# Optimization experiments

Hardware: AMD Instinct MI355X
Metric: run time of the kernel (lower is better)

## Reference

```python
import jax, jax.numpy as jnp
import numpy as np

EPS = 1e-4      # geomloss: eps = blur**p = 0.01**2
N_ITERS = 20    # fixed Sinkhorn iterations
UNI_T = 2.0     # uniformity temperature (Wang & Isola)


def _sqdist(x, y):
    # [N,D],[M,D] -> [N,M] squared euclidean distances
    return jnp.sum((x[:, None, :] - y[None, :, :]) ** 2, axis=-1)


def _cost(x, y):
    # geomloss p=2 cost: ||x-y||^2 / 2
    return 0.5 * _sqdist(x, y)


def _softmin(C, h):
    # f_i = -eps * log( (1/M) * sum_j exp((h_j - C_ij)/eps) )
    M = C.shape[1]
    lse = jax.nn.logsumexp((h[None, :] - C) / EPS, axis=1)
    return -EPS * (lse - jnp.log(jnp.float32(M)))


def _sinkhorn_potentials(C):
    # alternating log-domain Sinkhorn updates, uniform weights
    def body(carry, _):
        f, g = carry
        f = _softmin(C, g)
        g = _softmin(C.T, f)
        return (f, g), None
    init = (jnp.zeros(C.shape[0], C.dtype), jnp.zeros(C.shape[1], C.dtype))
    (f, g), _ = jax.lax.scan(body, init, None, length=N_ITERS)
    return f, g


def _sym_potential(C):
    # symmetric fixed-point for the debiasing terms OT_eps(a,a)
    def body(p, _):
        return 0.5 * (p + _softmin(C, p)), None
    p, _ = jax.lax.scan(body, jnp.zeros(C.shape[0], C.dtype), None, length=N_ITERS)
    return p


def sinkhorn_divergence(x, y):
    # debiased: S = OT(x,y) - 0.5*OT(x,x) - 0.5*OT(y,y); envelope-theorem grads
    Cxy = _cost(x, y)
    f_d, g_d = _sinkhorn_potentials(jax.lax.stop_gradient(Cxy))
    f = _softmin(Cxy, jax.lax.stop_gradient(g_d))          # final differentiable step
    g = _softmin(Cxy.T, jax.lax.stop_gradient(f_d))

    Cxx = _cost(x, x)
    px = _sym_potential(jax.lax.stop_gradient(Cxx))
    fx = _softmin(Cxx, jax.lax.stop_gradient(px))          # 0.5*OT(x,x) = mean(fx)

    Cyy = _cost(y, y)
    py = _sym_potential(jax.lax.stop_gradient(Cyy))
    fy = _softmin(Cyy, jax.lax.stop_gradient(py))

    return jnp.mean(f) + jnp.mean(g) - jnp.mean(fx) - jnp.mean(fy)


def uniformity(x):
    # log E_{i != j} [ exp(-t * ||x_i - x_j||^2) ]
    N = x.shape[0]
    D = _sqdist(x, x)
    D = D + jnp.diag(jnp.full((N,), jnp.inf, dtype=x.dtype))  # mask self-pairs
    return jax.nn.logsumexp(-UNI_T * D) - jnp.log(jnp.float32(N * (N - 1)))


def setup_inputs() -> dict:
    key = jax.random.key(0)
    k1, k2 = jax.random.split(key)
    p_q = jax.random.normal(k1, (4096, 3), dtype=jnp.float32)
    p_gt = jax.random.normal(k2, (4096, 4), dtype=jnp.float32)
    return {"p_q": p_q, "p_gt": p_gt}


def reference(p_q, p_gt):
    L = sinkhorn_divergence(p_q, p_gt[:, :3])
    L = L + uniformity(p_q)
    return L
```

## Files before the change

### kernel.cpp

```cpp
#include <hip/hip_runtime.h>

#define NPT  4096
#define NBLK 256
#define NTHR 1024

constexpr float EPSV   = 1e-4f;
constexpr float LN2F   = 0.69314718055994531f;
constexpr float E2     = EPSV * LN2F;
constexpr float INV_E2 = 1.0f / E2;
constexpr float S_U    = 4.0f / LN2F;

#define SMEM_FLOATS 34816
#define SMEM_BYTES  (SMEM_FLOATS * 4)

#define WF    0
#define WG    4096
#define WPX0  8192
#define WPX1  12288
#define WPY0  16384
#define WPY1  20480
#define WFFIN 24576
#define WFXV  28672
#define WFYV  32768
#define WULS  36864
#define WCTR  40960
#define WCNX  41984
#define WCNY  46080

__device__ __forceinline__ float fexp2(float x) { return __builtin_amdgcn_exp2f(x); }
__device__ __forceinline__ float flog2(float x) { return __builtin_amdgcn_logf(x); }

__device__ __forceinline__ float max3f(float a, float b, float c) {
    float d;
    asm("v_max3_f32 %0, %1, %2, %3" : "=v"(d) : "v"(a), "v"(b), "v"(c));
    return d;
}

template<int CTRL>
__device__ __forceinline__ float dppf(float x) {
    return __int_as_float(__builtin_amdgcn_update_dpp(
        __float_as_int(x), __float_as_int(x), CTRL, 0xF, 0xF, false));
}

__device__ __forceinline__ float gload(const float* p) {
    return __hip_atomic_load(p, __ATOMIC_RELAXED, __HIP_MEMORY_SCOPE_SYSTEM);
}
__device__ __forceinline__ void gstore(float* p, float v) {
    __hip_atomic_store(p, v, __ATOMIC_RELAXED, __HIP_MEMORY_SCOPE_SYSTEM);
}

__device__ __forceinline__ void group_barrier(unsigned* base, unsigned target, int b) {
    asm volatile("s_waitcnt vmcnt(0)" ::: "memory");
    __syncthreads();
    if (threadIdx.x == 0) {
        __hip_atomic_fetch_add(&base[(b & 15) * 16], 1u,
                               __ATOMIC_RELAXED, __HIP_MEMORY_SCOPE_SYSTEM);
        for (;;) {
            unsigned tot = 0;
#pragma unroll
            for (int i = 0; i < 16; ++i)
                tot += __hip_atomic_load(&base[i * 16],
                                         __ATOMIC_RELAXED, __HIP_MEMORY_SCOPE_SYSTEM);
            if (tot >= target) break;
            __builtin_amdgcn_s_sleep(1);
        }
    }
    __syncthreads();
}

template<bool ISU>
__device__ __forceinline__ void run_task(
    const float4* __restrict__ colpk, const float4* __restrict__ rowpk,
    int r0g, int half, int lane, float scale, float2* part2, int lr0)
{
    float xs0[4], xs1[4], xs2[4];
#pragma unroll
    for (int r = 0; r < 4; ++r) {
        float4 q = rowpk[r0g + r];
        xs0[r] = q.x * scale; xs1[r] = q.y * scale; xs2[r] = q.z * scale;
    }
    float m[4] = {-1e30f, -1e30f, -1e30f, -1e30f};
    float s[4] = {0.0f, 0.0f, 0.0f, 0.0f};
    const int cbase = half * 2048 + lane;
    const float4* col = colpk + cbase;
    int jbase = cbase;

#pragma unroll 1
    for (int chunk = 0; chunk < 8; ++chunk) {
        float av[4][4];
        float mc[4] = {-1e30f, -1e30f, -1e30f, -1e30f};
#pragma unroll
        for (int k = 0; k < 4; ++k) {
            const float4 c = col[k * 64];
#pragma unroll
            for (int r = 0; r < 4; ++r) {
                float a = fmaf(xs0[r], c.x, c.w);
                a = fmaf(xs1[r], c.y, a);
                a = fmaf(xs2[r], c.z, a);
                if (ISU) {
                    if (jbase + k * 64 == r0g + r) a = -1e30f;
                }
                av[r][k] = a;
                mc[r] = fmaxf(mc[r], a);
            }
        }
#pragma unroll
        for (int r = 0; r < 4; ++r) {
            float sc_ = fexp2(av[r][0] - mc[r]) + fexp2(av[r][1] - mc[r])
                      + fexp2(av[r][2] - mc[r]) + fexp2(av[r][3] - mc[r]);
            float dd = m[r] - mc[r];
            float e = fexp2(-fabsf(dd));
            float bigs   = (dd >= 0.0f) ? s[r] : sc_;
            float smalls = (dd >= 0.0f) ? sc_  : s[r];
            s[r] = fmaf(smalls, e, bigs);
            m[r] = fmaxf(m[r], mc[r]);
        }
        col += 256; jbase += 256;
    }
#pragma unroll
    for (int r = 0; r < 4; ++r) {
        const float ml = m[r];
        float mm = m[r];
        mm = fmaxf(mm, dppf<0xB1>(mm));
        mm = fmaxf(mm, dppf<0x4E>(mm));
        mm = fmaxf(mm, dppf<0x141>(mm));
        float ssv = s[r] * fexp2(ml - mm);
        ssv += dppf<0xB1>(ssv);
        ssv += dppf<0x4E>(ssv);
        ssv += dppf<0x141>(ssv);
        if ((lane & 7) == 0)
            part2[(lr0 + r) * 16 + half * 8 + (lane >> 3)] = make_float2(mm, ssv);
    }
}

__global__ void sink_init(const float* __restrict__ xin, const float* __restrict__ yin,
                          float* __restrict__ ws) {
    int t = blockIdx.x * blockDim.x + threadIdx.x;
    if (t < NPT) {
        gstore(ws + WF + t, 0.0f);
        gstore(ws + WG + t, 0.0f);
        gstore(ws + WPX0 + t, 0.0f);
        gstore(ws + WPY0 + t, 0.0f);
        float x0 = xin[3 * t], y0 = xin[3 * t + 1], z0 = xin[3 * t + 2];
        ws[WCNX + t] = 0.5f * (x0 * x0 + y0 * y0 + z0 * z0);
        float4 v = ((const float4*)yin)[t];
        ws[WCNY + t] = 0.5f * (v.x * v.x + v.y * v.y + v.z * v.z);
    }
    if (t < 512) {
        __hip_atomic_store((unsigned*)(ws + WCTR) + t, 0u,
                           __ATOMIC_RELAXED, __HIP_MEMORY_SCOPE_SYSTEM);
    }
}

__global__ __launch_bounds__(NTHR)
__attribute__((amdgpu_waves_per_eu(4, 4)))
void sink_main(
    const float* __restrict__ xin, const float* __restrict__ yin,
    float* __restrict__ ws, float* __restrict__ out)
{
    extern __shared__ float smem[];
    float4* packx = (float4*)smem;
    float4* packy = (float4*)(smem + 16384);
    float2* part2 = (float2*)(smem + 32768);

    float* f    = ws + WF;
    float* g    = ws + WG;
    float* px0  = ws + WPX0;
    float* px1  = ws + WPX1;
    float* py0  = ws + WPY0;
    float* py1  = ws + WPY1;
    float* ffin = ws + WFFIN;
    float* fxv  = ws + WFXV;
    float* fyv  = ws + WFYV;
    float* uls  = ws + WULS;
    unsigned* ctrA = (unsigned*)(ws + WCTR);
    unsigned* ctrB = (unsigned*)(ws + WCTR) + 256;
    const float* cnx = ws + WCNX;
    const float* cny = ws + WCNY;

    const int tid  = threadIdx.x;
    const int b    = blockIdx.x;
    const int wave = tid >> 6;
    const int lane = tid & 63;
    unsigned* cbarrier = (b < 128) ? ctrA : ctrB;

    for (int i = tid; i < NPT; i += NTHR) {
        packx[i] = make_float4(xin[3 * i], xin[3 * i + 1], xin[3 * i + 2], 0.0f);
        float4 v = ((const float4*)yin)[i];
        packy[i] = make_float4(v.x, v.y, v.z, 0.0f);
    }
    __syncthreads();

    for (int h = 0; h <= 40; ++h) {
        bool rows_x, cols_x, isU = false, avg = false;
        const float* pot; float* outp; float scale = INV_E2;
        int row0g, rows_pb;
        if (h == 0) {
            if (b < 128)      { rows_x = true;  cols_x = false; pot = g;    outp = f;    rows_pb = 32; row0g = b * 32; }
            else if (b < 192) { rows_x = true;  cols_x = true;  pot = px0;  outp = px1;  avg = true; rows_pb = 64; row0g = (b - 128) * 64; }
            else              { rows_x = true;  cols_x = true;  pot = nullptr; outp = uls; isU = true; scale = S_U; rows_pb = 64; row0g = (b - 192) * 64; }
        } else if (h == 40) {
            if (b < 128)      { rows_x = true;  cols_x = false; pot = g;    outp = ffin; rows_pb = 32; row0g = b * 32; }
            else if (b < 192) { rows_x = true;  cols_x = true;  pot = px0;  outp = fxv;  rows_pb = 64; row0g = (b - 128) * 64; }
            else              { rows_x = false; cols_x = false; pot = py0;  outp = fyv;  rows_pb = 64; row0g = (b - 192) * 64; }
        } else if (h & 1) {
            int k = (h - 1) >> 1;
            if (b < 128) { rows_x = false; cols_x = true;  pot = f; outp = g; rows_pb = 32; row0g = b * 32; }
            else         { rows_x = false; cols_x = false; pot = (k & 1) ? py1 : py0; outp = (k & 1) ? py0 : py1; avg = true; rows_pb = 32; row0g = (b - 128) * 32; }
        } else {
            int k = h >> 1;
            if (b < 128) { rows_x = true; cols_x = false; pot = g; outp = f; rows_pb = 32; row0g = b * 32; }
            else         { rows_x = true; cols_x = true;  pot = (k & 1) ? px1 : px0; outp = (k & 1) ? px0 : px1; avg = true; rows_pb = 32; row0g = (b - 128) * 32; }
        }

        float4* colpk = cols_x ? packx : packy;
        const float* ccn = cols_x ? cnx : cny;
        for (int j = tid; j < NPT; j += NTHR) {
            float pv = pot ? gload(pot + j) : 0.0f;
            float cn = ccn[j];
            ((float*)&colpk[j])[3] = (pv - cn) * scale;
        }
        __syncthreads();

        const float4* rowpk = rows_x ? packx : packy;
        const int ntask = rows_pb >> 1;
        for (int t = wave; t < ntask; t += 16) {
            int grp = t >> 1, half = t & 1;
            int lr0 = grp << 2;
            int r0g = row0g + lr0;
            if (isU) run_task<true >(colpk, rowpk, r0g, half, lane, scale, part2, lr0);
            else     run_task<false>(colpk, rowpk, r0g, half, lane, scale, part2, lr0);
        }
        __syncthreads();

        const float* rcn = rows_x ? cnx : cny;
        if (tid < rows_pb) {
            float2 pv2[16];
#pragma unroll
            for (int q = 0; q < 16; ++q) pv2[q] = part2[tid * 16 + q];
            float mm = pv2[0].x;
#pragma unroll
            for (int q = 1; q < 15; q += 2) mm = max3f(mm, pv2[q].x, pv2[q + 1].x);
            mm = fmaxf(mm, pv2[15].x);
            float ss = 0.0f;
#pragma unroll
            for (int q = 0; q < 16; ++q) ss += pv2[q].y * fexp2(pv2[q].x - mm);
            int rg = row0g + tid;
            float rn = rcn[rg];
            float lse2 = mm + flog2(ss) - rn * scale;
            float val;
            if (isU) {
                val = lse2;
            } else {
                val = -E2 * (lse2 - 12.0f);
                if (avg) val = 0.5f * (gload(pot + rg) + val);
            }
            gstore(outp + rg, val);
        }

        group_barrier(cbarrier, 128u * (unsigned)(h + 1), b);
    }

    if (b == 0) {
        if (tid == 0) {
            for (;;) {
                unsigned tot = 0;
#pragma unroll
                for (int i = 0; i < 16; ++i)
                    tot += __hip_atomic_load(&ctrB[i * 16],
                                             __ATOMIC_RELAXED, __HIP_MEMORY_SCOPE_SYSTEM);
                if (tot >= 128u * 41u) break;
                __builtin_amdgcn_s_sleep(1);
            }
        }
        __syncthreads();

        float sf = 0.f, sg = 0.f, sx = 0.f, sy = 0.f, um = -1e30f, us = 0.f;
        for (int i = tid; i < NPT; i += NTHR) {
            sf += gload(ffin + i); sg += gload(g + i);
            sx += gload(fxv + i);  sy += gload(fyv + i);
            float v = gload(uls + i);
            float mn = fmaxf(um, v);
            us = us * fexp2(um - mn) + fexp2(v - mn);
            um = mn;
        }
#pragma unroll
        for (int off = 1; off < 64; off <<= 1) {
            sf += __shfl_xor(sf, off, 64);
            sg += __shfl_xor(sg, off, 64);
            sx += __shfl_xor(sx, off, 64);
            sy += __shfl_xor(sy, off, 64);
            float mo = __shfl_xor(um, off, 64);
            float so = __shfl_xor(us, off, 64);
            float mn = fmaxf(um, mo);
            us = us * fexp2(um - mn) + so * fexp2(mo - mn);
            um = mn;
        }
        __syncthreads();
        if (lane == 0) {
            float* red = smem;
            red[wave * 6 + 0] = sf; red[wave * 6 + 1] = sg; red[wave * 6 + 2] = sx;
            red[wave * 6 + 3] = sy; red[wave * 6 + 4] = um; red[wave * 6 + 5] = us;
        }
        __syncthreads();
        if (tid == 0) {
            float* red = smem;
            float Sf = 0, Sg = 0, Sx = 0, Sy = 0, Um = -1e30f, Us = 0;
            for (int w = 0; w < 16; ++w) {
                Sf += red[w * 6 + 0]; Sg += red[w * 6 + 1];
                Sx += red[w * 6 + 2]; Sy += red[w * 6 + 3];
                float mo = red[w * 6 + 4], so = red[w * 6 + 5];
                float mn = fmaxf(Um, mo);
                Us = Us * fexp2(Um - mn) + so * fexp2(mo - mn);
                Um = mn;
            }
            float mean = (Sf + Sg - Sx - Sy) * (1.0f / 4096.0f);
            float U = LN2F * (Um + flog2(Us)) - logf(4096.0f * 4095.0f);
            out[0] = mean + U;
        }
    }
}

extern "C" void kernel_launch(void* const* d_in, const int* in_sizes, int n_in,
                              void* d_out, int out_size, void* d_ws, size_t ws_size,
                              hipStream_t stream) {
    const float* x = (const float*)d_in[0];
    const float* y = (const float*)d_in[1];
    float* ws  = (float*)d_ws;
    float* out = (float*)d_out;

    (void)hipFuncSetAttribute((const void*)sink_main,
                              hipFuncAttributeMaxDynamicSharedMemorySize, SMEM_BYTES);

    sink_init<<<4, 1024, 0, stream>>>(x, y, ws);
    sink_main<<<NBLK, NTHR, SMEM_BYTES, stream>>>(x, y, ws, out);
}
```

Baseline: 571.9 us.

## Use two-pass max-then-sum logsumexp with packed FP32 FMA over paired columns

Reorganises the shared-memory column layout so that two adjacent points are interleaved in float4 pairs, which allows v_pk_fma_f32 and v_pk_add_f32 to evaluate two cost entries per instruction. The online-rescaling logsumexp is replaced by two passes. The first pass computes the exact row maximum with a full-wavefront reduction, and the second sums exp2 values directly against that maximum, removing the per-chunk rescale exp and selects. In exchange, the FMA work and LDS column reads are done twice. The self-pair mask for the uniformity term is adapted to the paired layout.

```diff
diff --git a/kernel.cpp b/kernel.cpp
--- a/kernel.cpp
+++ b/kernel.cpp
@@ -27,9 +27,21 @@
 #define WCNX  41984
 #define WCNY  46080
 
+typedef float v2f __attribute__((ext_vector_type(2)));
+
 __device__ __forceinline__ float fexp2(float x) { return __builtin_amdgcn_exp2f(x); }
 __device__ __forceinline__ float flog2(float x) { return __builtin_amdgcn_logf(x); }
 
+__device__ __forceinline__ v2f pk_fma(v2f a, v2f b, v2f c) {
+    v2f d;
+    asm("v_pk_fma_f32 %0, %1, %2, %3" : "=v"(d) : "v"(a), "v"(b), "v"(c));
+    return d;
+}
+__device__ __forceinline__ v2f pk_add(v2f a, v2f b) {
+    v2f d;
+    asm("v_pk_add_f32 %0, %1, %2" : "=v"(d) : "v"(a), "v"(b));
+    return d;
+}
 __device__ __forceinline__ float max3f(float a, float b, float c) {
     float d;
     asm("v_max3_f32 %0, %1, %2, %3" : "=v"(d) : "v"(a), "v"(b), "v"(c));
@@ -70,66 +82,91 @@
 
 template<bool ISU>
 __device__ __forceinline__ void run_task(
-    const float4* __restrict__ colpk, const float4* __restrict__ rowpk,
+    const float4* __restrict__ cpA, const float4* __restrict__ cpB,
+    const float*  __restrict__ rAf, const float*  __restrict__ rBf,
     int r0g, int half, int lane, float scale, float2* part2, int lr0)
 {
-    float xs0[4], xs1[4], xs2[4];
+    v2f xs0[4], xs1[4], xs2[4];
 #pragma unroll
     for (int r = 0; r < 4; ++r) {
-        float4 q = rowpk[r0g + r];
-        xs0[r] = q.x * scale; xs1[r] = q.y * scale; xs2[r] = q.z * scale;
-    }
+        const int rr = r0g + r;
+        const int pb4 = (rr >> 1) * 4, c0 = rr & 1;
+        float xv = rAf[pb4 + c0] * scale;
+        float yv = rAf[pb4 + 2 + c0] * scale;
+        float zv = rBf[pb4 + c0] * scale;
+        xs0[r] = (v2f){xv, xv};
+        xs1[r] = (v2f){yv, yv};
+        xs2[r] = (v2f){zv, zv};
+    }
+    const int pbase = half * 1024 + lane;
+    const float4* cA = cpA + pbase;
+    const float4* cB = cpB + pbase;
+
     float m[4] = {-1e30f, -1e30f, -1e30f, -1e30f};
+#pragma unroll 2
+    for (int i = 0; i < 16; ++i) {
+        const float4 a4 = cA[i * 64];
+        const float4 b4 = cB[i * 64];
+        const v2f xx = {a4.x, a4.y}, yy = {a4.z, a4.w};
+        const v2f zz = {b4.x, b4.y}, gg = {b4.z, b4.w};
+#pragma unroll
+        for (int r = 0; r < 4; ++r) {
+            v2f a01 = pk_fma(xs2[r], zz, gg);
+            a01 = pk_fma(xs1[r], yy, a01);
+            a01 = pk_fma(xs0[r], xx, a01);
+            if (ISU) {
+                const int rr = r0g + r;
+                if (pbase + i * 64 == (rr >> 1)) {
+                    if (rr & 1) a01.y = -1e30f; else a01.x = -1e30f;
+                }
+            }
+            m[r] = max3f(m[r], a01.x, a01.y);
+        }
+    }
+#pragma unroll
+    for (int r = 0; r < 4; ++r) {
+        m[r] = fmaxf(m[r], dppf<0xB1>(m[r]));
+        m[r] = fmaxf(m[r], dppf<0x4E>(m[r]));
+        m[r] = fmaxf(m[r], dppf<0x141>(m[r]));
+        m[r] = fmaxf(m[r], dppf<0x140>(m[r]));
+        m[r] = fmaxf(m[r], __shfl_xor(m[r], 16, 64));
+        m[r] = fmaxf(m[r], __shfl_xor(m[r], 32, 64));
+    }
+    v2f nm[4];
+#pragma unroll
+    for (int r = 0; r < 4; ++r) nm[r] = (v2f){-m[r], -m[r]};
+
     float s[4] = {0.0f, 0.0f, 0.0f, 0.0f};
-    const int cbase = half * 2048 + lane;
-    const float4* col = colpk + cbase;
-    int jbase = cbase;
-
 #pragma unroll 1
-    for (int chunk = 0; chunk < 8; ++chunk) {
-        float av[4][4];
-        float mc[4] = {-1e30f, -1e30f, -1e30f, -1e30f};
-#pragma unroll
-        for (int k = 0; k < 4; ++k) {
-            const float4 c = col[k * 64];
-#pragma unroll
-            for (int r = 0; r < 4; ++r) {
-                float a = fmaf(xs0[r], c.x, c.w);
-                a = fmaf(xs1[r], c.y, a);
-                a = fmaf(xs2[r], c.z, a);
-                if (ISU) {
-                    if (jbase + k * 64 == r0g + r) a = -1e30f;
+    for (int i = 0; i < 16; ++i) {
+        const float4 a4 = cA[i * 64];
+        const float4 b4 = cB[i * 64];
+        const v2f xx = {a4.x, a4.y}, yy = {a4.z, a4.w};
+        const v2f zz = {b4.x, b4.y}, gg = {b4.z, b4.w};
+#pragma unroll
+        for (int r = 0; r < 4; ++r) {
+            v2f a01 = pk_fma(xs2[r], zz, gg);
+            a01 = pk_fma(xs1[r], yy, a01);
+            a01 = pk_fma(xs0[r], xx, a01);
+            if (ISU) {
+                const int rr = r0g + r;
+                if (pbase + i * 64 == (rr >> 1)) {
+                    if (rr & 1) a01.y = -1e30f; else a01.x = -1e30f;
                 }
-                av[r][k] = a;
-                mc[r] = fmaxf(mc[r], a);
-            }
-        }
-#pragma unroll
-        for (int r = 0; r < 4; ++r) {
-            float sc_ = fexp2(av[r][0] - mc[r]) + fexp2(av[r][1] - mc[r])
-                      + fexp2(av[r][2] - mc[r]) + fexp2(av[r][3] - mc[r]);
-            float dd = m[r] - mc[r];
-            float e = fexp2(-fabsf(dd));
-            float bigs   = (dd >= 0.0f) ? s[r] : sc_;
-            float smalls = (dd >= 0.0f) ? sc_  : s[r];
-            s[r] = fmaf(smalls, e, bigs);
-            m[r] = fmaxf(m[r], mc[r]);
-        }
-        col += 256; jbase += 256;
+            }
+            v2f d = pk_add(a01, nm[r]);
+            s[r] += fexp2(d.x);
+            s[r] += fexp2(d.y);
+        }
     }
 #pragma unroll
     for (int r = 0; r < 4; ++r) {
-        const float ml = m[r];
-        float mm = m[r];
-        mm = fmaxf(mm, dppf<0xB1>(mm));
-        mm = fmaxf(mm, dppf<0x4E>(mm));
-        mm = fmaxf(mm, dppf<0x141>(mm));
-        float ssv = s[r] * fexp2(ml - mm);
+        float ssv = s[r];
         ssv += dppf<0xB1>(ssv);
         ssv += dppf<0x4E>(ssv);
         ssv += dppf<0x141>(ssv);
         if ((lane & 7) == 0)
-            part2[(lr0 + r) * 16 + half * 8 + (lane >> 3)] = make_float2(mm, ssv);
+            part2[(lr0 + r) * 16 + half * 8 + (lane >> 3)] = make_float2(m[r], ssv);
     }
 }
 
@@ -159,8 +196,10 @@
     float* __restrict__ ws, float* __restrict__ out)
 {
     extern __shared__ float smem[];
-    float4* packx = (float4*)smem;
-    float4* packy = (float4*)(smem + 16384);
+    float4* pAx = (float4*)smem;
+    float4* pBx = (float4*)(smem + 8192);
+    float4* pAy = (float4*)(smem + 16384);
+    float4* pBy = (float4*)(smem + 24576);
     float2* part2 = (float2*)(smem + 32768);
 
     float* f    = ws + WF;
@@ -184,10 +223,15 @@
     const int lane = tid & 63;
     unsigned* cbarrier = (b < 128) ? ctrA : ctrB;
 
-    for (int i = tid; i < NPT; i += NTHR) {
-        packx[i] = make_float4(xin[3 * i], xin[3 * i + 1], xin[3 * i + 2], 0.0f);
-        float4 v = ((const float4*)yin)[i];
-        packy[i] = make_float4(v.x, v.y, v.z, 0.0f);
+    const float4* yin4 = (const float4*)yin;
+    for (int i = tid; i < 2048; i += NTHR) {
+        float x0 = xin[6 * i + 0], y0v = xin[6 * i + 1], z0 = xin[6 * i + 2];
+        float x1 = xin[6 * i + 3], y1v = xin[6 * i + 4], z1 = xin[6 * i + 5];
+        pAx[i] = make_float4(x0, x1, y0v, y1v);
+        pBx[i] = make_float4(z0, z1, 0.0f, 0.0f);
+        float4 v0 = yin4[2 * i], v1 = yin4[2 * i + 1];
+        pAy[i] = make_float4(v0.x, v1.x, v0.y, v1.y);
+        pBy[i] = make_float4(v0.z, v1.z, 0.0f, 0.0f);
     }
     __syncthreads();
 
@@ -213,23 +257,27 @@
             else         { rows_x = true; cols_x = true;  pot = (k & 1) ? px1 : px0; outp = (k & 1) ? px0 : px1; avg = true; rows_pb = 32; row0g = (b - 128) * 32; }
         }
 
-        float4* colpk = cols_x ? packx : packy;
+        float4* cpA = cols_x ? pAx : pAy;
+        float4* cpB = cols_x ? pBx : pBy;
         const float* ccn = cols_x ? cnx : cny;
-        for (int j = tid; j < NPT; j += NTHR) {
-            float pv = pot ? gload(pot + j) : 0.0f;
-            float cn = ccn[j];
-            ((float*)&colpk[j])[3] = (pv - cn) * scale;
-        }
-        __syncthreads();
-
-        const float4* rowpk = rows_x ? packx : packy;
+        for (int p = tid; p < 2048; p += NTHR) {
+            float2 cn2 = ((const float2*)ccn)[p];
+            float pv0 = pot ? gload(pot + 2 * p)     : 0.0f;
+            float pv1 = pot ? gload(pot + 2 * p + 1) : 0.0f;
+            ((float2*)&cpB[p])[1] = make_float2((pv0 - cn2.x) * scale,
+                                                (pv1 - cn2.y) * scale);
+        }
+        __syncthreads();
+
+        const float* rAf = (const float*)(cols_x == rows_x ? cpA : (rows_x ? pAx : pAy));
+        const float* rBf = (const float*)(cols_x == rows_x ? cpB : (rows_x ? pBx : pBy));
         const int ntask = rows_pb >> 1;
         for (int t = wave; t < ntask; t += 16) {
             int grp = t >> 1, half = t & 1;
             int lr0 = grp << 2;
             int r0g = row0g + lr0;
-            if (isU) run_task<true >(colpk, rowpk, r0g, half, lane, scale, part2, lr0);
-            else     run_task<false>(colpk, rowpk, r0g, half, lane, scale, part2, lr0);
+            if (isU) run_task<true >(cpA, cpB, rAf, rBf, r0g, half, lane, scale, part2, lr0);
+            else     run_task<false>(cpA, cpB, rAf, rBf, r0g, half, lane, scale, part2, lr0);
         }
         __syncthreads();
 
```

Measured after the change: 586.9 us. 2.6% more time.
